# Kernel tuning notes

Measured on AMD Instinct MI355X. Metric: run time of the kernel, lower is better.

## Reference

```python
import jax, jax.numpy as jnp
import numpy as np
import math

B, D, L = 32, 128, 512
NH = 8
DK = D // NH  # 16
DV = D // NH  # 16


def setup_inputs() -> dict:
    key = jax.random.key(0)
    kx, kq, kk, kv, ko = jax.random.split(key, 5)
    # xavier_normal std for [B, Dk, D] slabs: gain*sqrt(2/(fan_in+fan_out)) with fan over last two dims
    std_qkv = math.sqrt(2.0 / (DK + D))
    std_o = math.sqrt(2.0 / (DV * NH + D))
    x = jax.random.normal(kx, (B, D, L), dtype=jnp.float32)
    Wqs = jax.random.normal(kq, (NH, B, DK, D), dtype=jnp.float32) * std_qkv
    Wks = jax.random.normal(kk, (NH, B, DK, D), dtype=jnp.float32) * std_qkv
    Wvs = jax.random.normal(kv, (NH, B, DV, D), dtype=jnp.float32) * std_qkv
    Wo = jax.random.normal(ko, (B, DV * NH, D), dtype=jnp.float32) * std_o
    return {"x": x, "Wqs": Wqs, "Wks": Wks, "Wvs": Wvs, "Wo": Wo}


def reference(x, Wqs, Wks, Wvs, Wo):
    # x: [B, D, L]; Wqs/Wks: [NH, B, DK, D]; Wvs: [NH, B, DV, D]; Wo: [B, DV*NH, D]
    nh, b, dk, d = Wqs.shape
    l = x.shape[-1]
    inv_sqrt_dk = 1.0 / math.sqrt(dk)
    Q = jnp.einsum('nbkd,bdl->nbkl', Wqs, x)  # [NH, B, DK, L]
    K = jnp.einsum('nbkd,bdl->nbkl', Wks, x)  # [NH, B, DK, L]
    V = jnp.einsum('nbvd,bdl->nbvl', Wvs, x)  # [NH, B, DV, L]
    # scores[n,b,l,m] = sum_k Q[n,b,k,l]*K[n,b,k,m]; softmax over l (torch dim=1 of [B,L,L])
    scores = jnp.einsum('nbkl,nbkm->nblm', Q, K) * inv_sqrt_dk
    S = jax.nn.softmax(scores, axis=2)
    heads = jnp.einsum('nbvl,nblm->nbvm', V, S)  # [NH, B, DV, L]
    # .pop() in the original reverses head order before concatenation
    heads = heads[::-1]
    head = heads.transpose(1, 0, 2, 3).reshape(b, nh * heads.shape[2], l)  # [B, NH*DV, L]
    out = jnp.einsum('bod,bdl->bol', Wo, head)  # [B, D, L]
    return out
```

## Files before the change

### kernel.cpp

```cpp
#include <hip/hip_runtime.h>
#include <hip/hip_bf16.h>
#include <math.h>

#define B_   32
#define D_   128
#define L_   512
#define NH_  8
#define DK_  16

#define QKS  24
#define VST  520
#define XST  40

#define LOG2E 1.4426950408889634f
#define QSC   (0.25f * LOG2E)
#define SH2   (-11.541560327111707f)

typedef _Float16 h2 __attribute__((ext_vector_type(2)));
typedef _Float16 h4 __attribute__((ext_vector_type(4)));
typedef _Float16 h8 __attribute__((ext_vector_type(8)));
typedef __attribute__((ext_vector_type(4)))  float f32x4;
typedef __attribute__((ext_vector_type(16))) float f32x16;
typedef unsigned int u32x2 __attribute__((ext_vector_type(2)));
typedef unsigned int u32x4 __attribute__((ext_vector_type(4)));

__device__ __forceinline__ unsigned int cvt_pk_u(float a, float b) {
    return __builtin_bit_cast(unsigned int, __builtin_amdgcn_cvt_pkrtz(a, b));
}

#define MFMA_K32(a, b, c) __builtin_amdgcn_mfma_f32_16x16x32_f16((a), (b), (c), 0, 0, 0)
#define MFMA_32(a, b, c)  __builtin_amdgcn_mfma_f32_32x32x16_f16((a), (b), (c), 0, 0, 0)

__global__ __launch_bounds__(512, 2) void attn_mfma(
    const float* __restrict__ x,
    const float* __restrict__ Wq,
    const float* __restrict__ Wk,
    const float* __restrict__ Wv,
    _Float16* __restrict__ Ht)
{
    __shared__ __attribute__((aligned(16))) _Float16 T32a[512 * XST];
    __shared__ __attribute__((aligned(16))) _Float16 T32b[512 * XST];
    __shared__ __attribute__((aligned(16))) _Float16 Qh[512 * QKS];
    __shared__ __attribute__((aligned(16))) _Float16 Kh[512 * QKS];
    __shared__ __attribute__((aligned(16))) _Float16 Vs[16 * VST];

    const int nb = blockIdx.x;
    const int n  = nb >> 5;
    const int b  = nb & 31;
    const int t  = threadIdx.x;
    const int wv = t >> 6;
    const int ln = t & 63;
    const int l16 = ln & 15;
    const int g4  = ln >> 4;
    const int lm  = ln & 31;
    const int hi  = ln >> 5;

    const float* xb = x + (size_t)b * D_ * L_;
    const size_t woff = (size_t)(n * B_ + b) * DK_ * D_;
    const float* pWq = Wq + woff;
    const float* pWk = Wk + woff;
    const float* pWv = Wv + woff;

    const int sdd = (t >> 7) * 8;
    const int sl0 = (t & 127) * 4;

    #define STAGE(ks_, buf_)                                                   \
    {                                                                          \
        f32x4 xv[8];                                                           \
        _Pragma("unroll")                                                      \
        for (int j = 0; j < 8; ++j)                                            \
            xv[j] = *(const f32x4*)&xb[(size_t)((ks_) * 32 + sdd + j) * L_ + sl0]; \
        _Pragma("unroll")                                                      \
        for (int i = 0; i < 4; ++i) {                                          \
            h8 w;                                                              \
            _Pragma("unroll")                                                  \
            for (int j = 0; j < 8; ++j) w[j] = (_Float16)xv[j][i];             \
            *(h8*)&(buf_)[(sl0 + i) * XST + sdd] = w;                          \
        }                                                                      \
    }

    f32x4 Qa[4], Ka[4], Va[4];
    #pragma unroll
    for (int lt = 0; lt < 4; ++lt) {
        Qa[lt] = (f32x4){0.f,0.f,0.f,0.f};
        Ka[lt] = (f32x4){0.f,0.f,0.f,0.f};
        Va[lt] = (f32x4){0.f,0.f,0.f,0.f};
    }

    STAGE(0, T32a);
    __syncthreads();

    #pragma unroll
    for (int ks = 0; ks < 4; ++ks) {
        _Float16* cur = (ks & 1) ? T32b : T32a;
        _Float16* nxt = (ks & 1) ? T32a : T32b;
        if (ks < 3) STAGE(ks + 1, nxt);

        const int d0 = ks * 32 + g4 * 8;
        const float* aq = pWq + l16 * D_ + d0;
        const float* ak = pWk + l16 * D_ + d0;
        const float* av = pWv + l16 * D_ + d0;
        const f32x4 q0 = *(const f32x4*)aq, q1 = *(const f32x4*)(aq + 4);
        const f32x4 k0 = *(const f32x4*)ak, k1 = *(const f32x4*)(ak + 4);
        const f32x4 v0 = *(const f32x4*)av, v1 = *(const f32x4*)(av + 4);
        h8 Aq, Ak, Av;
        #pragma unroll
        for (int j = 0; j < 4; ++j) {
            Aq[j] = (_Float16)q0[j]; Aq[j + 4] = (_Float16)q1[j];
            Ak[j] = (_Float16)k0[j]; Ak[j + 4] = (_Float16)k1[j];
            Av[j] = (_Float16)v0[j]; Av[j + 4] = (_Float16)v1[j];
        }
        #pragma unroll
        for (int lt = 0; lt < 4; ++lt) {
            const int l = wv * 64 + lt * 16 + l16;
            const h8 Bx = *(const h8*)&cur[l * XST + g4 * 8];
            Qa[lt] = MFMA_K32(Aq, Bx, Qa[lt]);
            Ka[lt] = MFMA_K32(Ak, Bx, Ka[lt]);
            Va[lt] = MFMA_K32(Av, Bx, Va[lt]);
        }
        __syncthreads();
    }

    #pragma unroll
    for (int lt = 0; lt < 4; ++lt) {
        const int l = wv * 64 + lt * 16 + l16;
        h4 qv, kv;
        #pragma unroll
        for (int r = 0; r < 4; ++r) {
            qv[r] = (_Float16)(Qa[lt][r] * QSC);
            kv[r] = (_Float16)Ka[lt][r];
            Vs[(g4 * 4 + r) * VST + l] = (_Float16)Va[lt][r];
        }
        *(h4*)&Qh[l * QKS + g4 * 4] = qv;
        *(h4*)&Kh[l * QKS + g4 * 4] = kv;
    }
    __syncthreads();

    const int m0 = wv * 64;
    const h8 Bk0 = *(const h8*)&Kh[(m0 + lm) * QKS + 8 * hi];
    const h8 Bk1 = *(const h8*)&Kh[(m0 + 32 + lm) * QKS + 8 * hi];

    f32x16 shiftacc, pv0, pv1;
    #pragma unroll
    for (int i = 0; i < 16; ++i) { shiftacc[i] = SH2; pv0[i] = 0.f; pv1[i] = 0.f; }

    const bool vsel = (lm < 16);
    const int  vrow = lm & 15;
    const h8 ones8 = {(_Float16)1.f,(_Float16)1.f,(_Float16)1.f,(_Float16)1.f,
                      (_Float16)1.f,(_Float16)1.f,(_Float16)1.f,(_Float16)1.f};

    #pragma unroll 2
    for (int t32 = 0; t32 < 16; ++t32) {
        const int lb = t32 * 32;
        const h8 Aq2  = *(const h8*)&Qh[(lb + lm) * QKS + 8 * hi];
        const h8 Bv1r = *(const h8*)&Vs[vrow * VST + lb + 8 * hi];
        const h8 Bv2r = *(const h8*)&Vs[vrow * VST + lb + 16 + 8 * hi];
        const h8 Bv1 = vsel ? Bv1r : ones8;
        const h8 Bv2 = vsel ? Bv2r : ones8;

        const f32x16 sc0 = MFMA_32(Aq2, Bk0, shiftacc);
        const f32x16 sc1 = MFMA_32(Aq2, Bk1, shiftacc);

        float pA[16], pB[16];
        #pragma unroll
        for (int r = 0; r < 16; ++r) pA[r] = __builtin_amdgcn_exp2f(sc0[r]);
        #pragma unroll
        for (int r = 0; r < 16; ++r) pB[r] = __builtin_amdgcn_exp2f(sc1[r]);

        const unsigned int a0 = cvt_pk_u(pA[0],  pA[1]);
        const unsigned int a1 = cvt_pk_u(pA[2],  pA[3]);
        const unsigned int a2 = cvt_pk_u(pA[4],  pA[5]);
        const unsigned int a3 = cvt_pk_u(pA[6],  pA[7]);
        const unsigned int a4 = cvt_pk_u(pA[8],  pA[9]);
        const unsigned int a5 = cvt_pk_u(pA[10], pA[11]);
        const unsigned int a6 = cvt_pk_u(pA[12], pA[13]);
        const unsigned int a7 = cvt_pk_u(pA[14], pA[15]);
        const unsigned int b0 = cvt_pk_u(pB[0],  pB[1]);
        const unsigned int b1 = cvt_pk_u(pB[2],  pB[3]);
        const unsigned int b2 = cvt_pk_u(pB[4],  pB[5]);
        const unsigned int b3 = cvt_pk_u(pB[6],  pB[7]);
        const unsigned int b4 = cvt_pk_u(pB[8],  pB[9]);
        const unsigned int b5 = cvt_pk_u(pB[10], pB[11]);
        const unsigned int b6 = cvt_pk_u(pB[12], pB[13]);
        const unsigned int b7 = cvt_pk_u(pB[14], pB[15]);

        const u32x2 sA02 = __builtin_amdgcn_permlane32_swap(a0, a2, false, false);
        const u32x2 sA13 = __builtin_amdgcn_permlane32_swap(a1, a3, false, false);
        const u32x2 sA46 = __builtin_amdgcn_permlane32_swap(a4, a6, false, false);
        const u32x2 sA57 = __builtin_amdgcn_permlane32_swap(a5, a7, false, false);
        const u32x2 sB02 = __builtin_amdgcn_permlane32_swap(b0, b2, false, false);
        const u32x2 sB13 = __builtin_amdgcn_permlane32_swap(b1, b3, false, false);
        const u32x2 sB46 = __builtin_amdgcn_permlane32_swap(b4, b6, false, false);
        const u32x2 sB57 = __builtin_amdgcn_permlane32_swap(b5, b7, false, false);
        const h8 A1m0 = __builtin_bit_cast(h8, (u32x4){sA02.x, sA13.x, sA02.y, sA13.y});
        const h8 A2m0 = __builtin_bit_cast(h8, (u32x4){sA46.x, sA57.x, sA46.y, sA57.y});
        const h8 A1m1 = __builtin_bit_cast(h8, (u32x4){sB02.x, sB13.x, sB02.y, sB13.y});
        const h8 A2m1 = __builtin_bit_cast(h8, (u32x4){sB46.x, sB57.x, sB46.y, sB57.y});

        pv0 = MFMA_32(A1m0, Bv1, pv0);
        pv0 = MFMA_32(A2m0, Bv2, pv0);
        pv1 = MFMA_32(A1m1, Bv1, pv1);
        pv1 = MFMA_32(A2m1, Bv2, pv1);
    }

    const int kk = (NH_ - 1 - n) * 16 + l16;
    const int zlane = 16 + 32 * hi;
    _Float16* Hb = Ht + (size_t)b * 512 * 128;
    #pragma unroll
    for (int r = 0; r < 16; ++r) {
        const int mrow = (r & 3) + 8 * (r >> 2) + 4 * hi;
        const float zr0 = __shfl(pv0[r], zlane);
        const float zr1 = __shfl(pv1[r], zlane);
        const float rz0 = __builtin_amdgcn_rcpf(zr0);
        const float rz1 = __builtin_amdgcn_rcpf(zr1);
        if (lm < 16) {
            Hb[(size_t)(m0 + mrow) * 128 + kk]      = (_Float16)(pv0[r] * rz0);
            Hb[(size_t)(m0 + 32 + mrow) * 128 + kk] = (_Float16)(pv1[r] * rz1);
        }
    }
}

__global__ __launch_bounds__(256, 2) void out_proj_mfma(
    const float* __restrict__ Wo,
    const _Float16* __restrict__ Ht,
    float* __restrict__ out)
{
    const int ct = blockIdx.x;
    const int b  = blockIdx.y;
    const int t  = threadIdx.x;
    const int wv = t >> 6;
    const int ln = t & 63;
    const int l16 = ln & 15;
    const int g4  = ln >> 4;
    const int col0 = ct * 32;

    const float* Wb = Wo + (size_t)b * D_ * D_;
    const _Float16* Hb = Ht + (size_t)b * 512 * 128;

    f32x4 acc[2][2];
    #pragma unroll
    for (int mt = 0; mt < 2; ++mt)
        #pragma unroll
        for (int nt = 0; nt < 2; ++nt) acc[mt][nt] = (f32x4){0.f,0.f,0.f,0.f};

    #pragma unroll
    for (int ks = 0; ks < 4; ++ks) {
        const int k0 = ks * 32 + g4 * 8;
        h8 Ah[2];
        #pragma unroll
        for (int mt = 0; mt < 2; ++mt) {
            const float* ap = Wb + (size_t)(wv * 32 + mt * 16 + l16) * D_ + k0;
            const f32x4 w0 = *(const f32x4*)ap, w1 = *(const f32x4*)(ap + 4);
            #pragma unroll
            for (int j = 0; j < 4; ++j) {
                Ah[mt][j] = (_Float16)w0[j]; Ah[mt][j + 4] = (_Float16)w1[j];
            }
        }
        h8 Bh[2];
        #pragma unroll
        for (int nt = 0; nt < 2; ++nt)
            Bh[nt] = *(const h8*)&Hb[(size_t)(col0 + nt * 16 + l16) * 128 + k0];
        #pragma unroll
        for (int mt = 0; mt < 2; ++mt)
            #pragma unroll
            for (int nt = 0; nt < 2; ++nt)
                acc[mt][nt] = MFMA_K32(Ah[mt], Bh[nt], acc[mt][nt]);
    }

    float* ob = out + (size_t)b * D_ * L_;
    #pragma unroll
    for (int mt = 0; mt < 2; ++mt) {
        #pragma unroll
        for (int nt = 0; nt < 2; ++nt) {
            #pragma unroll
            for (int r = 0; r < 4; ++r) {
                ob[(size_t)(wv * 32 + mt * 16 + g4 * 4 + r) * L_ + col0 + nt * 16 + l16]
                    = acc[mt][nt][r];
            }
        }
    }
}

extern "C" void kernel_launch(void* const* d_in, const int* in_sizes, int n_in,
                              void* d_out, int out_size, void* d_ws, size_t ws_size,
                              hipStream_t stream)
{
    const float* x  = (const float*)d_in[0];
    const float* Wq = (const float*)d_in[1];
    const float* Wk = (const float*)d_in[2];
    const float* Wv = (const float*)d_in[3];
    const float* Wo = (const float*)d_in[4];
    float* out = (float*)d_out;

    _Float16* Ht = (_Float16*)d_ws;

    attn_mfma<<<dim3(NH_ * B_), dim3(512), 0, stream>>>(x, Wq, Wk, Wv, Ht);
    out_proj_mfma<<<dim3(16, B_), dim3(256), 0, stream>>>(Wo, Ht, out);
}
```

Before: 34.97 us.

## Split attention softmax reduction across two wave groups with 1024-thread blocks

Doubles the attention block to 1024 threads. In the projection phase each wave handles 32 positions instead of 64. In the attention phase the two wave halves each cover half of the l range and produce partial P·V and normaliser sums. The upper half writes its partials into shared memory that reuses the staging buffers, and the lower half adds them before normalising and storing. This gives each block more waves to hide latency, since the grid of 256 blocks gives only about one block per CU, at the cost of an extra barrier and an LDS exchange.

```diff
diff --git a/kernel.cpp b/kernel.cpp
--- a/kernel.cpp
+++ b/kernel.cpp
@@ -11,6 +11,7 @@
 #define QKS  24
 #define VST  520
 #define XST  40
+#define CST  34
 
 #define LOG2E 1.4426950408889634f
 #define QSC   (0.25f * LOG2E)
@@ -19,6 +20,7 @@
 typedef _Float16 h2 __attribute__((ext_vector_type(2)));
 typedef _Float16 h4 __attribute__((ext_vector_type(4)));
 typedef _Float16 h8 __attribute__((ext_vector_type(8)));
+typedef __attribute__((ext_vector_type(2)))  float f32x2;
 typedef __attribute__((ext_vector_type(4)))  float f32x4;
 typedef __attribute__((ext_vector_type(16))) float f32x16;
 typedef unsigned int u32x2 __attribute__((ext_vector_type(2)));
@@ -31,24 +33,29 @@
 #define MFMA_K32(a, b, c) __builtin_amdgcn_mfma_f32_16x16x32_f16((a), (b), (c), 0, 0, 0)
 #define MFMA_32(a, b, c)  __builtin_amdgcn_mfma_f32_32x32x16_f16((a), (b), (c), 0, 0, 0)
 
-__global__ __launch_bounds__(512, 2) void attn_mfma(
+__global__ __launch_bounds__(1024) void attn_mfma(
     const float* __restrict__ x,
     const float* __restrict__ Wq,
     const float* __restrict__ Wk,
     const float* __restrict__ Wv,
     _Float16* __restrict__ Ht)
 {
-    __shared__ __attribute__((aligned(16))) _Float16 T32a[512 * XST];
-    __shared__ __attribute__((aligned(16))) _Float16 T32b[512 * XST];
+    __shared__ __attribute__((aligned(16))) unsigned char SMEM[2 * 512 * XST * 2];
     __shared__ __attribute__((aligned(16))) _Float16 Qh[512 * QKS];
     __shared__ __attribute__((aligned(16))) _Float16 Kh[512 * QKS];
     __shared__ __attribute__((aligned(16))) _Float16 Vs[16 * VST];
+
+    _Float16* T32a = (_Float16*)SMEM;
+    _Float16* T32b = T32a + 512 * XST;
+    float*    comb = (float*)SMEM;
 
     const int nb = blockIdx.x;
     const int n  = nb >> 5;
     const int b  = nb & 31;
     const int t  = threadIdx.x;
     const int wv = t >> 6;
+    const int mwv   = wv & 7;
+    const int lhalf = wv >> 3;
     const int ln = t & 63;
     const int l16 = ln & 15;
     const int g4  = ln >> 4;
@@ -61,27 +68,27 @@
     const float* pWk = Wk + woff;
     const float* pWv = Wv + woff;
 
-    const int sdd = (t >> 7) * 8;
+    const int sdd = (t >> 7) * 4;
     const int sl0 = (t & 127) * 4;
 
     #define STAGE(ks_, buf_)                                                   \
     {                                                                          \
-        f32x4 xv[8];                                                           \
+        f32x4 xv[4];                                                           \
         _Pragma("unroll")                                                      \
-        for (int j = 0; j < 8; ++j)                                            \
+        for (int j = 0; j < 4; ++j)                                            \
             xv[j] = *(const f32x4*)&xb[(size_t)((ks_) * 32 + sdd + j) * L_ + sl0]; \
         _Pragma("unroll")                                                      \
         for (int i = 0; i < 4; ++i) {                                          \
-            h8 w;                                                              \
+            h4 w;                                                              \
             _Pragma("unroll")                                                  \
-            for (int j = 0; j < 8; ++j) w[j] = (_Float16)xv[j][i];             \
-            *(h8*)&(buf_)[(sl0 + i) * XST + sdd] = w;                          \
+            for (int j = 0; j < 4; ++j) w[j] = (_Float16)xv[j][i];             \
+            *(h4*)&(buf_)[(sl0 + i) * XST + sdd] = w;                          \
         }                                                                      \
     }
 
-    f32x4 Qa[4], Ka[4], Va[4];
-    #pragma unroll
-    for (int lt = 0; lt < 4; ++lt) {
+    f32x4 Qa[2], Ka[2], Va[2];
+    #pragma unroll
+    for (int lt = 0; lt < 2; ++lt) {
         Qa[lt] = (f32x4){0.f,0.f,0.f,0.f};
         Ka[lt] = (f32x4){0.f,0.f,0.f,0.f};
         Va[lt] = (f32x4){0.f,0.f,0.f,0.f};
@@ -111,8 +118,8 @@
             Av[j] = (_Float16)v0[j]; Av[j + 4] = (_Float16)v1[j];
         }
         #pragma unroll
-        for (int lt = 0; lt < 4; ++lt) {
-            const int l = wv * 64 + lt * 16 + l16;
+        for (int lt = 0; lt < 2; ++lt) {
+            const int l = wv * 32 + lt * 16 + l16;
             const h8 Bx = *(const h8*)&cur[l * XST + g4 * 8];
             Qa[lt] = MFMA_K32(Aq, Bx, Qa[lt]);
             Ka[lt] = MFMA_K32(Ak, Bx, Ka[lt]);
@@ -122,8 +129,8 @@
     }
 
     #pragma unroll
-    for (int lt = 0; lt < 4; ++lt) {
-        const int l = wv * 64 + lt * 16 + l16;
+    for (int lt = 0; lt < 2; ++lt) {
+        const int l = wv * 32 + lt * 16 + l16;
         h4 qv, kv;
         #pragma unroll
         for (int r = 0; r < 4; ++r) {
@@ -136,7 +143,7 @@
     }
     __syncthreads();
 
-    const int m0 = wv * 64;
+    const int m0 = mwv * 64;
     const h8 Bk0 = *(const h8*)&Kh[(m0 + lm) * QKS + 8 * hi];
     const h8 Bk1 = *(const h8*)&Kh[(m0 + 32 + lm) * QKS + 8 * hi];
 
@@ -149,8 +156,9 @@
     const h8 ones8 = {(_Float16)1.f,(_Float16)1.f,(_Float16)1.f,(_Float16)1.f,
                       (_Float16)1.f,(_Float16)1.f,(_Float16)1.f,(_Float16)1.f};
 
+    const int t32lo = lhalf * 8;
     #pragma unroll 2
-    for (int t32 = 0; t32 < 16; ++t32) {
+    for (int t32 = t32lo; t32 < t32lo + 8; ++t32) {
         const int lb = t32 * 32;
         const h8 Aq2  = *(const h8*)&Qh[(lb + lm) * QKS + 8 * hi];
         const h8 Bv1r = *(const h8*)&Vs[vrow * VST + lb + 8 * hi];
@@ -203,19 +211,38 @@
         pv1 = MFMA_32(A2m1, Bv2, pv1);
     }
 
-    const int kk = (NH_ - 1 - n) * 16 + l16;
-    const int zlane = 16 + 32 * hi;
-    _Float16* Hb = Ht + (size_t)b * 512 * 128;
-    #pragma unroll
-    for (int r = 0; r < 16; ++r) {
-        const int mrow = (r & 3) + 8 * (r >> 2) + 4 * hi;
-        const float zr0 = __shfl(pv0[r], zlane);
-        const float zr1 = __shfl(pv1[r], zlane);
-        const float rz0 = __builtin_amdgcn_rcpf(zr0);
-        const float rz1 = __builtin_amdgcn_rcpf(zr1);
-        if (lm < 16) {
-            Hb[(size_t)(m0 + mrow) * 128 + kk]      = (_Float16)(pv0[r] * rz0);
-            Hb[(size_t)(m0 + 32 + mrow) * 128 + kk] = (_Float16)(pv1[r] * rz1);
+    const int slot = mwv * 64 + ln;
+    if (lhalf == 1) {
+        #pragma unroll
+        for (int r = 0; r < 16; r += 2) {
+            *(f32x2*)&comb[slot * CST + r]      = (f32x2){pv0[r], pv0[r + 1]};
+            *(f32x2*)&comb[slot * CST + 16 + r] = (f32x2){pv1[r], pv1[r + 1]};
+        }
+    }
+    __syncthreads();
+    if (lhalf == 0) {
+        #pragma unroll
+        for (int r = 0; r < 16; r += 2) {
+            const f32x2 c0 = *(const f32x2*)&comb[slot * CST + r];
+            const f32x2 c1 = *(const f32x2*)&comb[slot * CST + 16 + r];
+            pv0[r] += c0[0]; pv0[r + 1] += c0[1];
+            pv1[r] += c1[0]; pv1[r + 1] += c1[1];
+        }
+
+        const int kk = (NH_ - 1 - n) * 16 + l16;
+        const int zlane = 16 + 32 * hi;
+        _Float16* Hb = Ht + (size_t)b * 512 * 128;
+        #pragma unroll
+        for (int r = 0; r < 16; ++r) {
+            const int mrow = (r & 3) + 8 * (r >> 2) + 4 * hi;
+            const float zr0 = __shfl(pv0[r], zlane);
+            const float zr1 = __shfl(pv1[r], zlane);
+            const float rz0 = __builtin_amdgcn_rcpf(zr0);
+            const float rz1 = __builtin_amdgcn_rcpf(zr1);
+            if (lm < 16) {
+                Hb[(size_t)(m0 + mrow) * 128 + kk]      = (_Float16)(pv0[r] * rz0);
+                Hb[(size_t)(m0 + 32 + mrow) * 128 + kk] = (_Float16)(pv1[r] * rz1);
+            }
         }
     }
 }
@@ -294,6 +321,6 @@
 
     _Float16* Ht = (_Float16*)d_ws;
 
-    attn_mfma<<<dim3(NH_ * B_), dim3(512), 0, stream>>>(x, Wq, Wk, Wv, Ht);
+    attn_mfma<<<dim3(NH_ * B_), dim3(1024), 0, stream>>>(x, Wq, Wk, Wv, Ht);
     out_proj_mfma<<<dim3(16, B_), dim3(256), 0, stream>>>(Wo, Ht, out);
 }
```

Result: slower. 39.44 us (+12.8%).

## Swizzle x staging in LDS and stage head output for coalesced per-head stores

Applied to the files above, without the earlier changes.

XOR-swizzles the column offset of the fp16 x tile in shared memory on both the write and the MFMA read side, to cut LDS bank conflicts. The attention epilogue now writes normalized head values into a small per-wave LDS tile (reusing the staging buffer) and then emits contiguous 8-byte vector stores. These go to a new head-major intermediate layout [B][NH][L][16] instead of scattered 2-byte stores into [B][L][128]. The output projection kernel is updated to read this new layout. The risk is the extra LDS round trip, and reusing the staging buffer relies on it being dead by this point.

```diff
diff --git a/kernel.cpp b/kernel.cpp
--- a/kernel.cpp
+++ b/kernel.cpp
@@ -11,6 +11,7 @@
 #define QKS  24
 #define VST  520
 #define XST  40
+#define ETS  20
 
 #define LOG2E 1.4426950408889634f
 #define QSC   (0.25f * LOG2E)
@@ -38,11 +39,13 @@
     const float* __restrict__ Wv,
     _Float16* __restrict__ Ht)
 {
-    __shared__ __attribute__((aligned(16))) _Float16 T32a[512 * XST];
-    __shared__ __attribute__((aligned(16))) _Float16 T32b[512 * XST];
+    __shared__ __attribute__((aligned(16))) unsigned char SMEM[2 * 512 * XST * 2];
     __shared__ __attribute__((aligned(16))) _Float16 Qh[512 * QKS];
     __shared__ __attribute__((aligned(16))) _Float16 Kh[512 * QKS];
     __shared__ __attribute__((aligned(16))) _Float16 Vs[16 * VST];
+
+    _Float16* T32a = (_Float16*)SMEM;
+    _Float16* T32b = T32a + 512 * XST;
 
     const int nb = blockIdx.x;
     const int n  = nb >> 5;
@@ -61,8 +64,9 @@
     const float* pWk = Wk + woff;
     const float* pWv = Wv + woff;
 
-    const int sdd = (t >> 7) * 8;
-    const int sl0 = (t & 127) * 4;
+    const int sdd  = (t >> 7) * 8;
+    const int sl0  = (t & 127) * 4;
+    const int sxor = ((t & 127) & 3) << 3;
 
     #define STAGE(ks_, buf_)                                                   \
     {                                                                          \
@@ -75,7 +79,7 @@
             h8 w;                                                              \
             _Pragma("unroll")                                                  \
             for (int j = 0; j < 8; ++j) w[j] = (_Float16)xv[j][i];             \
-            *(h8*)&(buf_)[(sl0 + i) * XST + sdd] = w;                          \
+            *(h8*)&(buf_)[(sl0 + i) * XST + (sdd ^ sxor)] = w;                 \
         }                                                                      \
     }
 
@@ -113,7 +117,7 @@
         #pragma unroll
         for (int lt = 0; lt < 4; ++lt) {
             const int l = wv * 64 + lt * 16 + l16;
-            const h8 Bx = *(const h8*)&cur[l * XST + g4 * 8];
+            const h8 Bx = *(const h8*)&cur[l * XST + ((g4 * 8) ^ ((((l) >> 2) & 3) << 3))];
             Qa[lt] = MFMA_K32(Aq, Bx, Qa[lt]);
             Ka[lt] = MFMA_K32(Ak, Bx, Ka[lt]);
             Va[lt] = MFMA_K32(Av, Bx, Va[lt]);
@@ -203,9 +207,8 @@
         pv1 = MFMA_32(A2m1, Bv2, pv1);
     }
 
-    const int kk = (NH_ - 1 - n) * 16 + l16;
+    _Float16* ET = ((_Float16*)SMEM) + wv * 64 * ETS;
     const int zlane = 16 + 32 * hi;
-    _Float16* Hb = Ht + (size_t)b * 512 * 128;
     #pragma unroll
     for (int r = 0; r < 16; ++r) {
         const int mrow = (r & 3) + 8 * (r >> 2) + 4 * hi;
@@ -214,10 +217,22 @@
         const float rz0 = __builtin_amdgcn_rcpf(zr0);
         const float rz1 = __builtin_amdgcn_rcpf(zr1);
         if (lm < 16) {
-            Hb[(size_t)(m0 + mrow) * 128 + kk]      = (_Float16)(pv0[r] * rz0);
-            Hb[(size_t)(m0 + 32 + mrow) * 128 + kk] = (_Float16)(pv1[r] * rz1);
-        }
-    }
+            ET[mrow * ETS + lm]        = (_Float16)(pv0[r] * rz0);
+            ET[(mrow + 32) * ETS + lm] = (_Float16)(pv1[r] * rz1);
+        }
+    }
+    asm volatile("s_waitcnt lgkmcnt(0)" ::: "memory");
+    __builtin_amdgcn_sched_barrier(0);
+
+    _Float16* Hb2 = Ht + (((size_t)b * NH_ + (NH_ - 1 - n)) * 512 + (m0 + ln)) * 16;
+    const h4 e0 = *(const h4*)&ET[ln * ETS + 0];
+    const h4 e1 = *(const h4*)&ET[ln * ETS + 4];
+    const h4 e2 = *(const h4*)&ET[ln * ETS + 8];
+    const h4 e3 = *(const h4*)&ET[ln * ETS + 12];
+    *(h4*)&Hb2[0]  = e0;
+    *(h4*)&Hb2[4]  = e1;
+    *(h4*)&Hb2[8]  = e2;
+    *(h4*)&Hb2[12] = e3;
 }
 
 __global__ __launch_bounds__(256, 2) void out_proj_mfma(
@@ -235,7 +250,7 @@
     const int col0 = ct * 32;
 
     const float* Wb = Wo + (size_t)b * D_ * D_;
-    const _Float16* Hb = Ht + (size_t)b * 512 * 128;
+    const _Float16* Hb = Ht + (size_t)b * NH_ * 512 * 16;
 
     f32x4 acc[2][2];
     #pragma unroll
@@ -246,6 +261,8 @@
     #pragma unroll
     for (int ks = 0; ks < 4; ++ks) {
         const int k0 = ks * 32 + g4 * 8;
+        const int hh = k0 >> 4;
+        const int kr = k0 & 15;
         h8 Ah[2];
         #pragma unroll
         for (int mt = 0; mt < 2; ++mt) {
@@ -259,7 +276,7 @@
         h8 Bh[2];
         #pragma unroll
         for (int nt = 0; nt < 2; ++nt)
-            Bh[nt] = *(const h8*)&Hb[(size_t)(col0 + nt * 16 + l16) * 128 + k0];
+            Bh[nt] = *(const h8*)&Hb[((size_t)hh * 512 + col0 + nt * 16 + l16) * 16 + kr];
         #pragma unroll
         for (int mt = 0; mt < 2; ++mt)
             #pragma unroll
```

New measurement: 34.17 us (median of 2 runs). 2.3% less time.
